# Kernel tuning notes

Hardware: AMD Instinct MI355X
Metric: run time of the kernel (lower is better)

Reference implementation:

```python
import jax, jax.numpy as jnp
import numpy as np

BINS = 64

def _histc_rows(flat, bins):
    # flat: [N, L]; per-row torch.histc semantics with min=max=0 (use data min/max)
    lo = flat.min(axis=1, keepdims=True)
    hi = flat.max(axis=1, keepdims=True)
    same = hi == lo
    lo = jnp.where(same, lo - 1.0, lo)
    hi = jnp.where(same, hi + 1.0, hi)
    # bin index; value == hi maps to bins -> clipped into last bin (torch includes max)
    idx = jnp.floor((flat - lo) / (hi - lo) * bins).astype(jnp.int32)
    idx = jnp.clip(idx, 0, bins - 1)
    n = flat.shape[0]
    flat_idx = idx + (jnp.arange(n, dtype=jnp.int32)[:, None] * bins)
    hist = jnp.zeros((n * bins,), dtype=flat.dtype).at[flat_idx.ravel()].add(1.0)
    return hist.reshape(n, bins)

def reference(x, conv_w, conv_b, head_w, head_b):
    # Conv2d(1 -> C, k=3, valid), NCHW
    y = jax.lax.conv_general_dilated(
        x, conv_w, window_strides=(1, 1), padding='VALID',
        dimension_numbers=('NCHW', 'OIHW', 'NCHW'))
    y = y + conv_b[None, :, None, None]
    y = jax.nn.relu(y)
    b, c, h, w = y.shape
    hist = _histc_rows(y.reshape(b * c, h * w), BINS)  # [B*C, bins]
    feat = hist.reshape(b, c * BINS)
    return feat @ head_w.T + head_b

def setup_inputs() -> dict:
    key = jax.random.key(0)
    k1, k2, k3, k4, k5 = jax.random.split(key, 5)
    C, K, F = 64, 3, 1000
    return {
        'x': jax.random.normal(k1, (64, 1, 256, 256), dtype=jnp.float32),
        'conv_w': jax.random.normal(k2, (C, 1, K, K), dtype=jnp.float32) * 0.1,
        'conv_b': jax.random.normal(k3, (C,), dtype=jnp.float32) * 0.1,
        'head_w': jax.random.normal(k4, (F, C * BINS), dtype=jnp.float32) * 0.02,
        'head_b': jax.random.normal(k5, (F,), dtype=jnp.float32) * 0.02,
    }
```

## Files before the change

kernel.cpp:

```cpp
#include <hip/hip_runtime.h>


typedef short bf16x8 __attribute__((ext_vector_type(8)));
typedef float f32x16 __attribute__((ext_vector_type(16)));
typedef float f32x2 __attribute__((ext_vector_type(2)));

#define TPITCH 35
#define F_OUT_ 1000
#define KDIM_ 4096

__device__ __forceinline__ unsigned f2bf(float f) {
    unsigned u = __float_as_uint(f);
    return (u + 0x7FFFu + ((u >> 16) & 1u)) >> 16;
}
__device__ __forceinline__ float bf2f(unsigned h) { return __uint_as_float(h << 16); }

__device__ __forceinline__ unsigned cvt_u32_sat(float f) {
    unsigned r;
    asm volatile("v_cvt_u32_f32 %0, %1" : "=v"(r) : "v"(f));
    return r;
}

union FragU { uint4 u; bf16x8 v; };

__global__ __launch_bounds__(512, 6) void conv_minmax_kernel(
    const float* __restrict__ x, const float* __restrict__ cw,
    const float* __restrict__ cb, float* __restrict__ featQ,
    float* __restrict__ mnbuf, float* __restrict__ mxbuf)
{
    __shared__ unsigned t32[256 * TPITCH];
    __shared__ float red[1024];

    const int tid = threadIdx.x;
    const int lane = tid & 63;
    const int w = __builtin_amdgcn_readfirstlane(tid >> 6);
    const int b = blockIdx.x;
    const int seg = blockIdx.y;
    const int mrow = lane & 31;
    const int kg = lane >> 5;
    const int r0 = seg * 32;
    const int vlim = min(32, 254 - r0);

    featQ[(seg * 64 + b) * 512 + tid] = 0.f;

    FragU bwh[2], bwl[2];
#pragma unroll
    for (int g = 0; g < 2; ++g) {
        int och = g * 32 + mrow;
        unsigned hh[8], ll[8];
#pragma unroll
        for (int j = 0; j < 8; ++j) {
            int k = kg * 8 + j, dr = k >> 2, dc = k & 3;
            float wv = (kg == 1 && j == 7) ? cb[och]
                     : ((dr < 3 && dc < 3) ? cw[och * 9 + dr * 3 + dc] : 0.f);
            unsigned h = f2bf(wv);
            hh[j] = h;
            ll[j] = f2bf(wv - bf2f(h));
        }
        bwh[g].u = make_uint4(hh[0] | (hh[1] << 16), hh[2] | (hh[3] << 16),
                              hh[4] | (hh[5] << 16), hh[6] | (hh[7] << 16));
        bwl[g].u = make_uint4(ll[0] | (ll[1] << 16), ll[2] | (ll[3] << 16),
                              ll[4] | (ll[5] << 16), ll[6] | (ll[7] << 16));
    }
    f32x16 zc;
#pragma unroll
    for (int r = 0; r < 16; ++r) zc[r] = 0.f;

    const float* xb = x + (size_t)b * 65536;
    for (int i = tid; i < TPITCH * 256; i += 512) {
        int lrow = i >> 8, col = i & 255;
        int grow = r0 + lrow;
        float v = (grow < 256) ? xb[grow * 256 + col] : 0.f;
        unsigned h = f2bf(v);
        unsigned l = f2bf(v - bf2f(h));
        t32[col * TPITCH + lrow] = (l << 16) | h;
    }
    __syncthreads();

    f32x2 mn2A = {3.4e38f, 3.4e38f}, mx2A = {-3.4e38f, -3.4e38f};
    f32x2 mn2B = {3.4e38f, 3.4e38f}, mx2B = {-3.4e38f, -3.4e38f};
    const int cbase = w * 32;
    const int cend = min(cbase + 32, 254);
    const unsigned* tb = t32 + mrow + 2 * kg;
    unsigned a0 = tb[cbase * TPITCH],       r1a = tb[cbase * TPITCH + 1];
    unsigned a1 = tb[(cbase + 1) * TPITCH], r1b = tb[(cbase + 1) * TPITCH + 1];
#pragma unroll 2
    for (int c = cbase; c < cend; ++c) {
        unsigned a2 = tb[(c + 2) * TPITCH];
        unsigned r1c = tb[(c + 2) * TPITCH + 1];
        FragU ah, al;
        ah.u = make_uint4(__builtin_amdgcn_perm(a1, a0, 0x05040100u), a2,
                          __builtin_amdgcn_perm(r1b, r1a, 0x05040100u),
                          (r1c & 0xFFFFu) | 0x3F800000u);
        al.u = make_uint4(__builtin_amdgcn_perm(a1, a0, 0x07060302u), a2 >> 16,
                          __builtin_amdgcn_perm(r1b, r1a, 0x07060302u), r1c >> 16);
        a0 = a1; a1 = a2; r1a = r1b; r1b = r1c;
        f32x16 accA = __builtin_amdgcn_mfma_f32_32x32x16_bf16(ah.v, bwh[0].v, zc, 0, 0, 0);
        f32x16 accB = __builtin_amdgcn_mfma_f32_32x32x16_bf16(ah.v, bwh[1].v, zc, 0, 0, 0);
        accA = __builtin_amdgcn_mfma_f32_32x32x16_bf16(al.v, bwh[0].v, accA, 0, 0, 0);
        accB = __builtin_amdgcn_mfma_f32_32x32x16_bf16(al.v, bwh[1].v, accB, 0, 0, 0);
        accA = __builtin_amdgcn_mfma_f32_32x32x16_bf16(ah.v, bwl[0].v, accA, 0, 0, 0);
        accB = __builtin_amdgcn_mfma_f32_32x32x16_bf16(ah.v, bwl[1].v, accB, 0, 0, 0);
        if (vlim >= 32) {
#pragma unroll
            for (int r = 0; r < 16; r += 2) {
                f32x2 vA = {accA[r], accA[r + 1]}, vB = {accB[r], accB[r + 1]};
                mn2A = __builtin_elementwise_min(mn2A, vA);
                mx2A = __builtin_elementwise_max(mx2A, vA);
                mn2B = __builtin_elementwise_min(mn2B, vB);
                mx2B = __builtin_elementwise_max(mx2B, vB);
            }
        } else {
#pragma unroll
            for (int r = 0; r < 16; ++r) {
                int crow = (r & 3) + 8 * (r >> 2) + 4 * kg;
                float vA = (crow < vlim) ? accA[r] : accA[0];
                float vB = (crow < vlim) ? accB[r] : accB[0];
                mn2A[0] = fminf(mn2A[0], vA); mx2A[0] = fmaxf(mx2A[0], vA);
                mn2B[0] = fminf(mn2B[0], vB); mx2B[0] = fmaxf(mx2B[0], vB);
            }
        }
    }

    float mnA = fminf(mn2A[0], mn2A[1]), mxA = fmaxf(mx2A[0], mx2A[1]);
    float mnB = fminf(mn2B[0], mn2B[1]), mxB = fmaxf(mx2B[0], mx2B[1]);
    mnA = fminf(mnA, __shfl_xor(mnA, 32, 64));
    mxA = fmaxf(mxA, __shfl_xor(mxA, 32, 64));
    mnB = fminf(mnB, __shfl_xor(mnB, 32, 64));
    mxB = fmaxf(mxB, __shfl_xor(mxB, 32, 64));
    __syncthreads();
    if (lane < 32) {
        red[w * 64 + mrow] = mnA;        red[512 + w * 64 + mrow] = mxA;
        red[w * 64 + 32 + mrow] = mnB;   red[512 + w * 64 + 32 + mrow] = mxB;
    }
    __syncthreads();
    if (tid < 64) {
        float a = red[tid], c = red[512 + tid];
#pragma unroll
        for (int i = 1; i < 8; ++i) {
            a = fminf(a, red[i * 64 + tid]);
            c = fmaxf(c, red[512 + i * 64 + tid]);
        }
        mnbuf[((b * 64 + tid) << 3) | seg] = a;
        mxbuf[((b * 64 + tid) << 3) | seg] = c;
    }
}

__global__ __launch_bounds__(512, 6) void conv_hist_kernel(
    const float* __restrict__ x, const float* __restrict__ cw,
    const float* __restrict__ cb, float* __restrict__ featQ,
    const float* __restrict__ mnbuf, const float* __restrict__ mxbuf)
{
    __shared__ unsigned t32[256 * TPITCH];
    __shared__ unsigned hist[65 * 32];

    const int tid = threadIdx.x;
    const int lane = tid & 63;
    const int w = __builtin_amdgcn_readfirstlane(tid >> 6);
    const int b = blockIdx.x;
    const int seg = blockIdx.y;
    const int gz = blockIdx.z;
    const int mrow = lane & 31;
    const int kg = lane >> 5;
    const int r0 = seg * 32;
    const int vlim = min(32, 254 - r0);
    const int och = gz * 32 + mrow;

    float rmn = 3.402823466e38f, rmx = -3.402823466e38f;
#pragma unroll
    for (int s = 0; s < 8; ++s) {
        rmn = fminf(rmn, mnbuf[((b * 64 + och) << 3) | s]);
        rmx = fmaxf(rmx, mxbuf[((b * 64 + och) << 3) | s]);
    }
    float lo = fmaxf(rmn, 0.f);
    float hi = fmaxf(rmx, 0.f);
    if (hi == lo) { lo -= 1.f; hi += 1.f; }
    const float sc = 63.984f / (hi - lo);
    const float nls = -lo * sc;
    for (int i = tid; i < 65 * 32; i += 512) hist[i] = 0u;

    FragU bwh, bwl;
    {
        unsigned hh[8], ll[8];
#pragma unroll
        for (int j = 0; j < 8; ++j) {
            int k = kg * 8 + j, dr = k >> 2, dc = k & 3;
            float wv = (kg == 1 && j == 7) ? fmaf(cb[och], sc, nls)
                     : ((dr < 3 && dc < 3) ? cw[och * 9 + dr * 3 + dc] * sc : 0.f);
            unsigned h = f2bf(wv);
            hh[j] = h;
            ll[j] = f2bf(wv - bf2f(h));
        }
        bwh.u = make_uint4(hh[0] | (hh[1] << 16), hh[2] | (hh[3] << 16),
                           hh[4] | (hh[5] << 16), hh[6] | (hh[7] << 16));
        bwl.u = make_uint4(ll[0] | (ll[1] << 16), ll[2] | (ll[3] << 16),
                           ll[4] | (ll[5] << 16), ll[6] | (ll[7] << 16));
    }
    f32x16 zc;
#pragma unroll
    for (int r = 0; r < 16; ++r) zc[r] = 0.f;

    const float* xb = x + (size_t)b * 65536;
    for (int i = tid; i < TPITCH * 256; i += 512) {
        int lrow = i >> 8, col = i & 255;
        int grow = r0 + lrow;
        float v = (grow < 256) ? xb[grow * 256 + col] : 0.f;
        unsigned h = f2bf(v);
        unsigned l = f2bf(v - bf2f(h));
        t32[col * TPITCH + lrow] = (l << 16) | h;
    }
    __syncthreads();

    const int cbase = w * 32;
    const int cend = min(cbase + 32, 254);
    unsigned* hrow = hist + mrow;
    const unsigned* tb = t32 + mrow + 2 * kg;
    unsigned a0 = tb[cbase * TPITCH],       r1a = tb[cbase * TPITCH + 1];
    unsigned a1 = tb[(cbase + 1) * TPITCH], r1b = tb[(cbase + 1) * TPITCH + 1];
#pragma unroll 2
    for (int c = cbase; c < cend; ++c) {
        unsigned a2 = tb[(c + 2) * TPITCH];
        unsigned r1c = tb[(c + 2) * TPITCH + 1];
        FragU ah, al;
        ah.u = make_uint4(__builtin_amdgcn_perm(a1, a0, 0x05040100u), a2,
                          __builtin_amdgcn_perm(r1b, r1a, 0x05040100u),
                          (r1c & 0xFFFFu) | 0x3F800000u);
        al.u = make_uint4(__builtin_amdgcn_perm(a1, a0, 0x07060302u), a2 >> 16,
                          __builtin_amdgcn_perm(r1b, r1a, 0x07060302u), r1c >> 16);
        a0 = a1; a1 = a2; r1a = r1b; r1b = r1c;
        f32x16 acc = __builtin_amdgcn_mfma_f32_32x32x16_bf16(ah.v, bwh.v, zc, 0, 0, 0);
        acc = __builtin_amdgcn_mfma_f32_32x32x16_bf16(al.v, bwh.v, acc, 0, 0, 0);
        acc = __builtin_amdgcn_mfma_f32_32x32x16_bf16(ah.v, bwl.v, acc, 0, 0, 0);
        if (vlim >= 32) {
#pragma unroll
            for (int r = 0; r < 16; ++r) {
                unsigned bin = cvt_u32_sat(acc[r]);
                atomicAdd(&hrow[bin << 5], 1u);
            }
        } else {
#pragma unroll
            for (int r = 0; r < 16; ++r) {
                int crow = (r & 3) + 8 * (r >> 2) + 4 * kg;
                unsigned bin = cvt_u32_sat(acc[r]);
                if (crow >= vlim) bin = 64u;
                atomicAdd(&hrow[bin << 5], 1u);
            }
        }
    }
    __syncthreads();

    for (int i = tid; i < 2048; i += 512) {
        int o = i >> 6, bin = i & 63;
        float cnt = (float)hist[(bin << 5) + o];
        int k = ((gz * 32 + o) << 6) | bin;
        atomicAdd(&featQ[((k >> 2) << 8) | (b << 2) | (k & 3)], cnt);
    }
}

__global__ __launch_bounds__(512) void head_kernel(
    const float* __restrict__ featQ, const float* __restrict__ hw,
    float* __restrict__ part)
{
    __shared__ float red[8][8][64];
    const int tid = threadIdx.x;
    const int m = tid & 63;
    const int kh = __builtin_amdgcn_readfirstlane(tid >> 6);
    const int n0 = blockIdx.x * 8;
    const int q = blockIdx.y;
    const int kqbase = q * 256 + kh * 32;
    const float* fb = featQ + kqbase * 256 + (m << 2);
    const float* wp[8];
#pragma unroll
    for (int c = 0; c < 8; ++c)
        wp[c] = hw + (size_t)(n0 + c) * KDIM_ + (kqbase << 2);

    float a[8] = {0.f, 0.f, 0.f, 0.f, 0.f, 0.f, 0.f, 0.f};
#pragma unroll 2
    for (int kq = 0; kq < 32; ++kq) {
        float4 f = *(const float4*)(fb + (kq << 8));
#pragma unroll
        for (int c = 0; c < 8; ++c) {
            float4 u = *(const float4*)(wp[c] + (kq << 2));
            a[c] += f.x * u.x + f.y * u.y + f.z * u.z + f.w * u.w;
        }
    }
#pragma unroll
    for (int c = 0; c < 8; ++c) red[kh][c][m] = a[c];
    __syncthreads();
    {
        int c = tid >> 6, mm = tid & 63;
        float v = 0.f;
#pragma unroll
        for (int j = 0; j < 8; ++j) v += red[j][c][mm];
        part[(size_t)q * 64000 + (n0 + c) * 64 + mm] = v;
    }
}

__global__ __launch_bounds__(256) void head_reduce_kernel(
    const float* __restrict__ part, const float* __restrict__ hb,
    float* __restrict__ out)
{
    int idx = blockIdx.x * 256 + threadIdx.x;
    int n = idx >> 6, m = idx & 63;
    float v = hb[n] + part[idx] + part[64000 + idx] +
              part[128000 + idx] + part[192000 + idx];
    out[(size_t)m * F_OUT_ + n] = v;
}

extern "C" void kernel_launch(void* const* d_in, const int* in_sizes, int n_in,
                              void* d_out, int out_size, void* d_ws, size_t ws_size,
                              hipStream_t stream) {
    const float* x      = (const float*)d_in[0];
    const float* conv_w = (const float*)d_in[1];
    const float* conv_b = (const float*)d_in[2];
    const float* head_w = (const float*)d_in[3];
    const float* head_b = (const float*)d_in[4];
    float* out   = (float*)d_out;
    float* featQ = (float*)d_ws;
    float* mnbuf = featQ + 262144;
    float* mxbuf = mnbuf + 32768;
    float* part  = mxbuf + 32768;

    dim3 g1(64, 8);
    dim3 g2(64, 8, 2);
    conv_minmax_kernel<<<g1, 512, 0, stream>>>(x, conv_w, conv_b, featQ, mnbuf, mxbuf);
    conv_hist_kernel<<<g2, 512, 0, stream>>>(x, conv_w, conv_b, featQ, mnbuf, mxbuf);
    head_kernel<<<dim3(125, 4), 512, 0, stream>>>(featQ, head_w, part);
    head_reduce_kernel<<<250, 256, 0, stream>>>(part, head_b, out);
}
```

Before: 186.3 us.

## Prefetch LDS fragments one step ahead, scalarize min/max, split head K into 16

The conv loops now load the next column's LDS words one iteration early, with a clamped index so the extra read stays inside the tile. This is meant to hide LDS latency behind the MFMAs. The min/max tracking drops the 2-wide vector type in favour of scalar fminf/fmaxf chains. The head GEMM is split 16 ways along K instead of 4, with 256-thread blocks, giving 2000 blocks for better occupancy; the cost is four times more partial sums that the reduce kernel must read.

```diff
diff --git a/kernel.cpp b/kernel.cpp
--- a/kernel.cpp
+++ b/kernel.cpp
@@ -3,7 +3,6 @@
 
 typedef short bf16x8 __attribute__((ext_vector_type(8)));
 typedef float f32x16 __attribute__((ext_vector_type(16)));
-typedef float f32x2 __attribute__((ext_vector_type(2)));
 
 #define TPITCH 35
 #define F_OUT_ 1000
@@ -77,24 +76,26 @@
     }
     __syncthreads();
 
-    f32x2 mn2A = {3.4e38f, 3.4e38f}, mx2A = {-3.4e38f, -3.4e38f};
-    f32x2 mn2B = {3.4e38f, 3.4e38f}, mx2B = {-3.4e38f, -3.4e38f};
+    float mnA = 3.4e38f, mxA = -3.4e38f;
+    float mnB = 3.4e38f, mxB = -3.4e38f;
     const int cbase = w * 32;
     const int cend = min(cbase + 32, 254);
     const unsigned* tb = t32 + mrow + 2 * kg;
     unsigned a0 = tb[cbase * TPITCH],       r1a = tb[cbase * TPITCH + 1];
     unsigned a1 = tb[(cbase + 1) * TPITCH], r1b = tb[(cbase + 1) * TPITCH + 1];
+    unsigned a2 = tb[(cbase + 2) * TPITCH], r1c = tb[(cbase + 2) * TPITCH + 1];
 #pragma unroll 2
     for (int c = cbase; c < cend; ++c) {
-        unsigned a2 = tb[(c + 2) * TPITCH];
-        unsigned r1c = tb[(c + 2) * TPITCH + 1];
+        int cp = min(c + 3, 255);
+        unsigned a3  = tb[cp * TPITCH];
+        unsigned r1d = tb[cp * TPITCH + 1];
         FragU ah, al;
         ah.u = make_uint4(__builtin_amdgcn_perm(a1, a0, 0x05040100u), a2,
                           __builtin_amdgcn_perm(r1b, r1a, 0x05040100u),
                           (r1c & 0xFFFFu) | 0x3F800000u);
         al.u = make_uint4(__builtin_amdgcn_perm(a1, a0, 0x07060302u), a2 >> 16,
                           __builtin_amdgcn_perm(r1b, r1a, 0x07060302u), r1c >> 16);
-        a0 = a1; a1 = a2; r1a = r1b; r1b = r1c;
+        a0 = a1; a1 = a2; a2 = a3; r1a = r1b; r1b = r1c; r1c = r1d;
         f32x16 accA = __builtin_amdgcn_mfma_f32_32x32x16_bf16(ah.v, bwh[0].v, zc, 0, 0, 0);
         f32x16 accB = __builtin_amdgcn_mfma_f32_32x32x16_bf16(ah.v, bwh[1].v, zc, 0, 0, 0);
         accA = __builtin_amdgcn_mfma_f32_32x32x16_bf16(al.v, bwh[0].v, accA, 0, 0, 0);
@@ -104,11 +105,10 @@
         if (vlim >= 32) {
 #pragma unroll
             for (int r = 0; r < 16; r += 2) {
-                f32x2 vA = {accA[r], accA[r + 1]}, vB = {accB[r], accB[r + 1]};
-                mn2A = __builtin_elementwise_min(mn2A, vA);
-                mx2A = __builtin_elementwise_max(mx2A, vA);
-                mn2B = __builtin_elementwise_min(mn2B, vB);
-                mx2B = __builtin_elementwise_max(mx2B, vB);
+                mnA = fminf(fminf(mnA, accA[r]), accA[r + 1]);
+                mxA = fmaxf(fmaxf(mxA, accA[r]), accA[r + 1]);
+                mnB = fminf(fminf(mnB, accB[r]), accB[r + 1]);
+                mxB = fmaxf(fmaxf(mxB, accB[r]), accB[r + 1]);
             }
         } else {
 #pragma unroll
@@ -116,14 +116,12 @@
                 int crow = (r & 3) + 8 * (r >> 2) + 4 * kg;
                 float vA = (crow < vlim) ? accA[r] : accA[0];
                 float vB = (crow < vlim) ? accB[r] : accB[0];
-                mn2A[0] = fminf(mn2A[0], vA); mx2A[0] = fmaxf(mx2A[0], vA);
-                mn2B[0] = fminf(mn2B[0], vB); mx2B[0] = fmaxf(mx2B[0], vB);
+                mnA = fminf(mnA, vA); mxA = fmaxf(mxA, vA);
+                mnB = fminf(mnB, vB); mxB = fmaxf(mxB, vB);
             }
         }
     }
 
-    float mnA = fminf(mn2A[0], mn2A[1]), mxA = fmaxf(mx2A[0], mx2A[1]);
-    float mnB = fminf(mn2B[0], mn2B[1]), mxB = fmaxf(mx2B[0], mx2B[1]);
     mnA = fminf(mnA, __shfl_xor(mnA, 32, 64));
     mxA = fmaxf(mxA, __shfl_xor(mxA, 32, 64));
     mnB = fminf(mnB, __shfl_xor(mnB, 32, 64));
@@ -217,17 +215,19 @@
     const unsigned* tb = t32 + mrow + 2 * kg;
     unsigned a0 = tb[cbase * TPITCH],       r1a = tb[cbase * TPITCH + 1];
     unsigned a1 = tb[(cbase + 1) * TPITCH], r1b = tb[(cbase + 1) * TPITCH + 1];
+    unsigned a2 = tb[(cbase + 2) * TPITCH], r1c = tb[(cbase + 2) * TPITCH + 1];
 #pragma unroll 2
     for (int c = cbase; c < cend; ++c) {
-        unsigned a2 = tb[(c + 2) * TPITCH];
-        unsigned r1c = tb[(c + 2) * TPITCH + 1];
+        int cp = min(c + 3, 255);
+        unsigned a3  = tb[cp * TPITCH];
+        unsigned r1d = tb[cp * TPITCH + 1];
         FragU ah, al;
         ah.u = make_uint4(__builtin_amdgcn_perm(a1, a0, 0x05040100u), a2,
                           __builtin_amdgcn_perm(r1b, r1a, 0x05040100u),
                           (r1c & 0xFFFFu) | 0x3F800000u);
         al.u = make_uint4(__builtin_amdgcn_perm(a1, a0, 0x07060302u), a2 >> 16,
                           __builtin_amdgcn_perm(r1b, r1a, 0x07060302u), r1c >> 16);
-        a0 = a1; a1 = a2; r1a = r1b; r1b = r1c;
+        a0 = a1; a1 = a2; a2 = a3; r1a = r1b; r1b = r1c; r1c = r1d;
         f32x16 acc = __builtin_amdgcn_mfma_f32_32x32x16_bf16(ah.v, bwh.v, zc, 0, 0, 0);
         acc = __builtin_amdgcn_mfma_f32_32x32x16_bf16(al.v, bwh.v, acc, 0, 0, 0);
         acc = __builtin_amdgcn_mfma_f32_32x32x16_bf16(ah.v, bwl.v, acc, 0, 0, 0);
@@ -257,17 +257,17 @@
     }
 }
 
-__global__ __launch_bounds__(512) void head_kernel(
+__global__ __launch_bounds__(256) void head_kernel(
     const float* __restrict__ featQ, const float* __restrict__ hw,
     float* __restrict__ part)
 {
-    __shared__ float red[8][8][64];
+    __shared__ float red[4][8][64];
     const int tid = threadIdx.x;
     const int m = tid & 63;
     const int kh = __builtin_amdgcn_readfirstlane(tid >> 6);
     const int n0 = blockIdx.x * 8;
     const int q = blockIdx.y;
-    const int kqbase = q * 256 + kh * 32;
+    const int kqbase = q * 64 + kh * 16;
     const float* fb = featQ + kqbase * 256 + (m << 2);
     const float* wp[8];
 #pragma unroll
@@ -276,7 +276,7 @@
 
     float a[8] = {0.f, 0.f, 0.f, 0.f, 0.f, 0.f, 0.f, 0.f};
 #pragma unroll 2
-    for (int kq = 0; kq < 32; ++kq) {
+    for (int kq = 0; kq < 16; ++kq) {
         float4 f = *(const float4*)(fb + (kq << 8));
 #pragma unroll
         for (int c = 0; c < 8; ++c) {
@@ -287,11 +287,9 @@
 #pragma unroll
     for (int c = 0; c < 8; ++c) red[kh][c][m] = a[c];
     __syncthreads();
-    {
-        int c = tid >> 6, mm = tid & 63;
-        float v = 0.f;
-#pragma unroll
-        for (int j = 0; j < 8; ++j) v += red[j][c][mm];
+    for (int s = tid; s < 512; s += 256) {
+        int c = s >> 6, mm = s & 63;
+        float v = red[0][c][mm] + red[1][c][mm] + red[2][c][mm] + red[3][c][mm];
         part[(size_t)q * 64000 + (n0 + c) * 64 + mm] = v;
     }
 }
@@ -302,8 +300,9 @@
 {
     int idx = blockIdx.x * 256 + threadIdx.x;
     int n = idx >> 6, m = idx & 63;
-    float v = hb[n] + part[idx] + part[64000 + idx] +
-              part[128000 + idx] + part[192000 + idx];
+    float v = hb[n];
+#pragma unroll
+    for (int q = 0; q < 16; ++q) v += part[q * 64000 + idx];
     out[(size_t)m * F_OUT_ + n] = v;
 }
 
@@ -325,6 +324,6 @@
     dim3 g2(64, 8, 2);
     conv_minmax_kernel<<<g1, 512, 0, stream>>>(x, conv_w, conv_b, featQ, mnbuf, mxbuf);
     conv_hist_kernel<<<g2, 512, 0, stream>>>(x, conv_w, conv_b, featQ, mnbuf, mxbuf);
-    head_kernel<<<dim3(125, 4), 512, 0, stream>>>(featQ, head_w, part);
+    head_kernel<<<dim3(125, 16), 256, 0, stream>>>(featQ, head_w, part);
     head_reduce_kernel<<<250, 256, 0, stream>>>(part, head_b, out);
 }
```

Measured after the change: 178.3 us. 4.3% less time.
